# Kernel optimization log

Hardware: AMD Instinct MI355X
Metric: run time of the kernel (lower is better)

The kernel has to match this reference:

```python
import jax, jax.numpy as jnp
import numpy as np

MARGIN = 0.3   # init margin
NUMBER = 1024  # OHEM: number of hardest losses to mine
N, D = 8192, 128


def setup_inputs() -> dict:
    key = jax.random.key(0)
    k1, k2 = jax.random.split(key)
    pair1 = jax.random.normal(k1, (N, D), dtype=jnp.float32)
    pair2 = jax.random.normal(k2, (N, D), dtype=jnp.float32)
    return {"pair1": pair1, "pair2": pair2}


def _pairwise_losses(pair1, pair2):
    # d[i, j] = ||pair1[i] - pair2[j]||^2 via GEMM expansion
    sq1 = jnp.sum(pair1 * pair1, axis=1)            # [N]
    sq2 = jnp.sum(pair2 * pair2, axis=1)            # [N]
    cross = pair1 @ pair2.T                          # [N, N]
    d = sq1[:, None] + sq2[None, :] - 2.0 * cross    # [N, N]
    dist_ap = jnp.diagonal(d)                        # [N], ||pair1[i]-pair2[i]||^2
    loss = jax.nn.relu(dist_ap[:, None] - d + MARGIN)  # [N, N]
    offdiag = ~jnp.eye(d.shape[0], dtype=bool)       # i == j is skipped
    return loss, offdiag


def reference(pair1, pair2):
    loss, offdiag = _pairwise_losses(pair1, pair2)
    n = loss.shape[0]
    cnt = 2 * n * (n - 1)  # original appends each (i, j) loss twice
    # all_loss: mean over all 2*N*(N-1) (duplicated) losses
    all_loss = 2.0 * jnp.sum(jnp.where(offdiag, loss, 0.0)) / cnt
    # OHEM: top NUMBER losses over the duplicated candidate set
    flat = jnp.where(offdiag, loss, -1.0).ravel()    # sentinel -1 masks diagonal
    flat2 = jnp.concatenate([flat, flat])            # each loss appears twice
    topv, _ = jax.lax.top_k(flat2, NUMBER)
    pos = topv > 0.0
    avg_num = jnp.sum(pos)
    avg_sum = jnp.sum(jnp.where(pos, topv, 0.0))
    # if no positive loss among the mined set, fall back to the single largest loss
    avg_loss = jnp.where(avg_num > 0, avg_sum / jnp.maximum(avg_num, 1).astype(topv.dtype), topv[0])
    return avg_loss, all_loss
```

## Files before the change

kernel.cpp:

```cpp
#include <hip/hip_runtime.h>
#include <stdint.h>


#define NROWS 8192
#define DDIM  128
#define MARGIN_F 0.3f
#define HALFK 512
#define SUBCAP 8192
#define SHIST_BINS 1024

typedef unsigned short u16;
typedef short bf16x8 __attribute__((ext_vector_type(8)));
typedef float f32x4 __attribute__((ext_vector_type(4)));

#define OFF_P1B  0
#define OFF_P2B  (2*1024*1024)
#define OFF_AARR (4*1024*1024)
#define OFF_BARR (OFF_AARR + 32768)
#define OFF_MISC (OFF_AARR + 65536)
#define OFF_CAND (OFF_MISC + 8192)

__device__ __forceinline__ u16 f2bf(float f) {
    unsigned int u = __float_as_uint(f);
    u = (u + 0x7FFFu + ((u >> 16) & 1u)) >> 16;
    return (u16)u;
}
__device__ __forceinline__ float bf2f(u16 u) {
    return __uint_as_float(((unsigned int)u) << 16);
}

__global__ __launch_bounds__(256) void prep_kernel(
    const float* __restrict__ p1, const float* __restrict__ p2,
    u16* __restrict__ p1b, u16* __restrict__ p2b,
    float* __restrict__ aArr, float* __restrict__ bArr,
    int* __restrict__ misc)
{
    if (blockIdx.x == 0) {
        for (int i = threadIdx.x; i < 1232; i += 256) misc[i] = 0;
    }
    const int wid = threadIdx.x >> 6, lane = threadIdx.x & 63;
    const int row = blockIdx.x*4 + wid;
    const float2 v1 = *(const float2*)&p1[row*DDIM + lane*2];
    const float2 v2 = *(const float2*)&p2[row*DDIM + lane*2];
    p1b[row*DDIM + lane*2]     = f2bf(v1.x);
    p1b[row*DDIM + lane*2 + 1] = f2bf(v1.y);
    p2b[row*DDIM + lane*2]     = f2bf(v2.x);
    p2b[row*DDIM + lane*2 + 1] = f2bf(v2.y);
    float sq = v2.x*v2.x + v2.y*v2.y;
    float cp = v1.x*v2.x + v1.y*v2.y;
    #pragma unroll
    for (int off = 32; off > 0; off >>= 1) {
        sq += __shfl_down(sq, off);
        cp += __shfl_down(cp, off);
    }
    if (lane == 0) {
        bArr[row] = sq;
        aArr[row] = sq - 2.0f*cp + MARGIN_F;
    }
}

__global__ __launch_bounds__(256) void sample_kernel(
    const u16* __restrict__ p1b, const u16* __restrict__ p2b,
    const float* __restrict__ aArr, const float* __restrict__ bArr,
    int* __restrict__ shist)
{
    __shared__ float p1row[DDIM];
    __shared__ int h[SHIST_BINS];
    const int b = blockIdx.x;
    const int i = (b >> 3)*1024 + 512;
    const int j0 = (b & 7)*1024;
    const int tid = threadIdx.x;
    for (int k = tid; k < SHIST_BINS; k += 256) h[k] = 0;
    if (tid < DDIM) p1row[tid] = bf2f(p1b[i*DDIM + tid]);
    __syncthreads();
    const float ai = aArr[i];
    #pragma unroll
    for (int jj = 0; jj < 4; ++jj) {
        const int j = j0 + jj*256 + tid;
        const u16* prow = &p2b[j*DDIM];
        float dot = 0.f;
        for (int k = 0; k < DDIM; k += 8) {
            uint4 q = *(const uint4*)&prow[k];
            const u16* e = (const u16*)&q;
            #pragma unroll
            for (int t = 0; t < 8; ++t) dot += p1row[k + t] * bf2f(e[t]);
        }
        float v = ai - bArr[j] + 2.0f*dot;
        if (j != i && v > 0.f) {
            int bin = (int)(v * 4.0f);
            if (bin > SHIST_BINS - 1) bin = SHIST_BINS - 1;
            atomicAdd(&h[bin], 1);
        }
    }
    __syncthreads();
    for (int k = tid; k < SHIST_BINS; k += 256) if (h[k]) atomicAdd(&shist[k], h[k]);
}

__global__ __launch_bounds__(256) void pick_kernel(
    const int* __restrict__ shist, float* __restrict__ Tv)
{
    __shared__ int h[SHIST_BINS];
    __shared__ int chunk[256];
    const int tid = threadIdx.x;
    #pragma unroll
    for (int k = 0; k < 4; ++k) h[tid + k*256] = shist[tid + k*256];
    __syncthreads();
    int cs = 0;
    #pragma unroll
    for (int k = 0; k < 4; ++k) cs += h[tid*4 + k];
    chunk[tid] = cs;
    __syncthreads();
    if (tid == 0) {
        int run = 0, tc = -1;
        for (int t = 255; t >= 0; --t) {
            if (run + chunk[t] >= 8) { tc = t; break; }
            run += chunk[t];
        }
        float t0 = 0.f;
        if (tc >= 0) {
            int b = tc*4 + 3;
            for (; b >= tc*4; --b) { run += h[b]; if (run >= 8) break; }
            if (b < tc*4) b = tc*4;
            while (run > 24 && run - h[b] >= 8 && b < SHIST_BINS - 1) { run -= h[b]; b++; }
            t0 = 0.25f * (float)b;
        }
        *Tv = t0;
    }
}

__global__ __launch_bounds__(512, 4) void pair_gemm(
    const u16* __restrict__ p1b, const u16* __restrict__ p2b,
    const float* __restrict__ aArr, const float* __restrict__ bArr,
    const float* __restrict__ Tv,
    float* __restrict__ pS, int* __restrict__ pP,
    int* __restrict__ candCnt, float* __restrict__ cand)
{
    __shared__ u16 At[128][136];
    __shared__ u16 Bt[128][136];
    __shared__ float sredS[8];
    __shared__ int   sredP[8];
    const int tid = threadIdx.x;
    const int bi = blockIdx.y, bj = blockIdx.x;
    const int i0 = bi*128, j0 = bj*128;
    const float T0 = *Tv;
    #pragma unroll
    for (int it = 0; it < 4; ++it) {
        int c = tid + it*512;
        int r = c >> 4, cc = (c & 15) * 8;
        *(uint4*)&At[r][cc] = *(const uint4*)&p1b[(i0 + r)*DDIM + cc];
        *(uint4*)&Bt[r][cc] = *(const uint4*)&p2b[(j0 + r)*DDIM + cc];
    }
    __syncthreads();
    const int lane = tid & 63, wid = tid >> 6;
    const int r16 = lane & 15, hi = lane >> 4;
    const int wm = (wid >> 2)*64;
    const int wn = (wid & 3)*32;
    f32x4 acc[4][2];
    #pragma unroll
    for (int a = 0; a < 4; ++a)
        #pragma unroll
        for (int b = 0; b < 2; ++b) acc[a][b] = (f32x4){0.f, 0.f, 0.f, 0.f};
    #pragma unroll
    for (int ks = 0; ks < 4; ++ks) {
        const int kc = ks*32 + hi*8;
        bf16x8 aF[4], bF[2];
        #pragma unroll
        for (int mi = 0; mi < 4; ++mi) aF[mi] = *(const bf16x8*)&At[wm + mi*16 + r16][kc];
        #pragma unroll
        for (int ni = 0; ni < 2; ++ni) bF[ni] = *(const bf16x8*)&Bt[wn + ni*16 + r16][kc];
        #pragma unroll
        for (int mi = 0; mi < 4; ++mi)
            #pragma unroll
            for (int ni = 0; ni < 2; ++ni)
                acc[mi][ni] = __builtin_amdgcn_mfma_f32_16x16x32_bf16(aF[mi], bF[ni], acc[mi][ni], 0, 0, 0);
    }
    float bv[2], av[4][4];
    #pragma unroll
    for (int ni = 0; ni < 2; ++ni) bv[ni] = bArr[j0 + wn + ni*16 + r16];
    #pragma unroll
    for (int mi = 0; mi < 4; ++mi)
        #pragma unroll
        for (int r = 0; r < 4; ++r) av[mi][r] = aArr[i0 + wm + mi*16 + hi*4 + r];
    const int copy = (bi ^ bj) & 63;
    int*   myCnt  = &candCnt[copy];
    float* myCand = &cand[(size_t)copy * SUBCAP];
    float lsum = 0.f; int pcnt = 0;
    #pragma unroll
    for (int mi = 0; mi < 4; ++mi) {
        #pragma unroll
        for (int ni = 0; ni < 2; ++ni) {
            const bool hasDiag = (i0 + wm + mi*16) == (j0 + wn + ni*16);
            #pragma unroll
            for (int r = 0; r < 4; ++r) {
                const float v = av[mi][r] - bv[ni] + 2.0f*acc[mi][ni][r];
                lsum += fmaxf(v, 0.f);
                pcnt += (v > 0.f) ? 1 : 0;
                bool ok = (v >= T0);
                if (hasDiag && (hi*4 + r) == r16) ok = false;
                if (ok) {
                    int idx = atomicAdd(myCnt, 1);
                    if (idx < SUBCAP) myCand[idx] = v;
                }
            }
        }
    }
    #pragma unroll
    for (int off = 32; off > 0; off >>= 1) {
        lsum += __shfl_down(lsum, off);
        pcnt += __shfl_down(pcnt, off);
    }
    if (lane == 0) { sredS[wid] = lsum; sredP[wid] = pcnt; }
    __syncthreads();
    if (tid == 0) {
        float s = 0.f; int p = 0;
        #pragma unroll
        for (int w = 0; w < 8; ++w) { s += sredS[w]; p += sredP[w]; }
        atomicAdd(&pS[copy], s);
        atomicAdd(&pP[copy], p);
    }
}

__device__ __forceinline__ float block_reduce1024(float v, float* red, int tid) {
    #pragma unroll
    for (int off = 32; off > 0; off >>= 1) v += __shfl_down(v, off);
    __syncthreads();
    if ((tid & 63) == 0) red[tid >> 6] = v;
    __syncthreads();
    if (tid == 0) {
        float t = 0.f;
        #pragma unroll
        for (int w = 0; w < 16; ++w) t += red[w];
        red[0] = t;
    }
    __syncthreads();
    return red[0];
}

__global__ __launch_bounds__(1024) void select_kernel(
    const float* __restrict__ pS, const int* __restrict__ pP,
    const int* __restrict__ candCnt, const float* __restrict__ cand,
    const float* __restrict__ Tv, float* __restrict__ out)
{
    __shared__ int h1[1024];
    __shared__ int h2[1024];
    __shared__ float red[16];
    __shared__ int ints[8];
    __shared__ float fl[2];
    __shared__ float lst[4096];
    const int tid = threadIdx.x;
    for (int k = tid; k < 1024; k += 1024) { h1[k] = 0; h2[k] = 0; }
    if (tid == 0) {
        double sd = 0.0; int p = 0, c = 0;
        for (int k = 0; k < 64; ++k) {
            sd += (double)pS[k];
            p += pP[k];
            int cc = candCnt[k];
            c += (cc > SUBCAP ? SUBCAP : cc);
        }
        sd -= (double)NROWS * (double)MARGIN_F;
        if (sd < 0.0) sd = 0.0;
        p -= NROWS;
        if (p < 0) p = 0;
        ints[0] = p; ints[1] = c; ints[6] = 0;
        fl[0] = (float)sd;
    }
    __syncthreads();
    const int P = ints[0], C = ints[1];
    const float S = fl[0];
    const float all_loss = S * (1.0f / 67100672.0f);
    const float lo = *Tv;
    float avg = 0.f;

    if (P == 0) {
        avg = 0.f;
    } else if (P < HALFK) {
        avg = S / (float)P;
    } else if (C < HALFK) {
        float s = 0.f;
        for (int c = 0; c < 64; ++c) {
            int n = min(candCnt[c], SUBCAP);
            for (int k = tid; k < n; k += 1024) s += cand[(size_t)c*SUBCAP + k];
        }
        s = block_reduce1024(s, red, tid);
        avg = (C > 0) ? (s + (float)(HALFK - C)*lo) / (float)HALFK : 0.f;
    } else {
        for (int c = 0; c < 64; ++c) {
            int n = min(candCnt[c], SUBCAP);
            for (int k = tid; k < n; k += 1024) {
                float v = cand[(size_t)c*SUBCAP + k];
                int b = (int)((v - lo) * 0.25f);
                b = b < 0 ? 0 : (b > 1023 ? 1023 : b);
                atomicAdd(&h1[b], 1);
            }
        }
        __syncthreads();
        if (tid == 0) {
            int run = 0;
            for (int b = 1023; b >= 0; --b) {
                run += h1[b];
                if (run >= HALFK) { ints[2] = b; ints[3] = HALFK - (run - h1[b]); break; }
            }
        }
        __syncthreads();
        const int b1 = ints[2], needK = ints[3];
        const float lo2 = lo + (float)b1 * 4.0f;
        float s1 = 0.f;
        for (int c = 0; c < 64; ++c) {
            int n = min(candCnt[c], SUBCAP);
            for (int k = tid; k < n; k += 1024) {
                float v = cand[(size_t)c*SUBCAP + k];
                int b = (int)((v - lo) * 0.25f);
                b = b < 0 ? 0 : (b > 1023 ? 1023 : b);
                if (b > b1) s1 += v;
                else if (b == b1) {
                    int sb = (int)((v - lo2) * 256.0f);
                    sb = sb < 0 ? 0 : (sb > 1023 ? 1023 : sb);
                    atomicAdd(&h2[sb], 1);
                }
            }
        }
        s1 = block_reduce1024(s1, red, tid);
        if (tid == 0) {
            int run = 0;
            for (int b = 1023; b >= 0; --b) {
                run += h2[b];
                if (run >= needK) { ints[4] = b; ints[5] = needK - (run - h2[b]); break; }
            }
        }
        __syncthreads();
        const int b2 = ints[4], need3 = ints[5];
        float s2 = 0.f;
        for (int c = 0; c < 64; ++c) {
            int n = min(candCnt[c], SUBCAP);
            for (int k = tid; k < n; k += 1024) {
                float v = cand[(size_t)c*SUBCAP + k];
                int b = (int)((v - lo) * 0.25f);
                b = b < 0 ? 0 : (b > 1023 ? 1023 : b);
                if (b == b1) {
                    int sb = (int)((v - lo2) * 256.0f);
                    sb = sb < 0 ? 0 : (sb > 1023 ? 1023 : sb);
                    if (sb > b2) s2 += v;
                    else if (sb == b2) {
                        int idx = atomicAdd(&ints[6], 1);
                        if (idx < 4096) lst[idx] = v;
                    }
                }
            }
        }
        s2 = block_reduce1024(s2, red, tid);
        __syncthreads();
        const int m = min(ints[6], 4096);
        float s3 = 0.f;
        for (int k = tid; k < m; k += 1024) {
            float v = lst[k]; int g = 0;
            for (int j = 0; j < m; ++j) {
                float u = lst[j];
                g += (u > v) || (u == v && j < k);
            }
            if (g < need3) s3 += v;
        }
        s3 = block_reduce1024(s3, red, tid);
        avg = (s1 + s2 + s3) * (1.0f / (float)HALFK);
    }
    if (tid == 0) { out[0] = avg; out[1] = all_loss; }
}

extern "C" void kernel_launch(void* const* d_in, const int* in_sizes, int n_in,
                              void* d_out, int out_size, void* d_ws, size_t ws_size,
                              hipStream_t stream)
{
    const float* p1 = (const float*)d_in[0];
    const float* p2 = (const float*)d_in[1];
    char* ws = (char*)d_ws;
    u16*   p1b  = (u16*)(ws + OFF_P1B);
    u16*   p2b  = (u16*)(ws + OFF_P2B);
    float* aArr = (float*)(ws + OFF_AARR);
    float* bArr = (float*)(ws + OFF_BARR);
    int*   misc = (int*)(ws + OFF_MISC);
    int*   shist = misc;
    float* pS   = (float*)(misc + 1024);
    int*   pP   = misc + 1088;
    int*   cCnt = misc + 1152;
    float* Tv   = (float*)(misc + 1216);
    float* cand = (float*)(ws + OFF_CAND);
    float* out  = (float*)d_out;

    prep_kernel<<<NROWS/4, 256, 0, stream>>>(p1, p2, p1b, p2b, aArr, bArr, misc);
    sample_kernel<<<64, 256, 0, stream>>>(p1b, p2b, aArr, bArr, shist);
    pick_kernel<<<1, 256, 0, stream>>>(shist, Tv);
    dim3 grid(64, 64);
    pair_gemm<<<grid, 512, 0, stream>>>(p1b, p2b, aArr, bArr, Tv, pS, pP, cCnt, cand);
    select_kernel<<<1, 1024, 0, stream>>>(pS, pP, cCnt, cand, Tv, out);
}
```

Before: 375.1 us.

## Fuse launches via last-block tickets and convert fp32 to bf16 inside the GEMM

Removes the separate bf16 conversion pass: the GEMM tiles now load fp32 inputs and round to bf16 while staging into shared memory, and the sampler reads fp32 directly. The pick kernel is folded into the sampler and the select kernel into the GEMM, each using an atomic ticket so the last finishing block runs the tail work, cutting two launches. The trade-off is double the global read bytes per GEMM tile, conversion work repeated by every tile, and a tail selection that now runs with 512 threads inside a register-constrained GEMM block.

```diff
diff --git a/kernel.cpp b/kernel.cpp
--- a/kernel.cpp
+++ b/kernel.cpp
@@ -8,13 +8,13 @@
 #define HALFK 512
 #define SUBCAP 8192
 #define SHIST_BINS 1024
+#define TICK_SAMP 1220
+#define TICK_GEMM 1224
 
 typedef unsigned short u16;
 typedef short bf16x8 __attribute__((ext_vector_type(8)));
 typedef float f32x4 __attribute__((ext_vector_type(4)));
 
-#define OFF_P1B  0
-#define OFF_P2B  (2*1024*1024)
 #define OFF_AARR (4*1024*1024)
 #define OFF_BARR (OFF_AARR + 32768)
 #define OFF_MISC (OFF_AARR + 65536)
@@ -25,65 +25,60 @@
     u = (u + 0x7FFFu + ((u >> 16) & 1u)) >> 16;
     return (u16)u;
 }
-__device__ __forceinline__ float bf2f(u16 u) {
-    return __uint_as_float(((unsigned int)u) << 16);
-}
 
 __global__ __launch_bounds__(256) void prep_kernel(
     const float* __restrict__ p1, const float* __restrict__ p2,
-    u16* __restrict__ p1b, u16* __restrict__ p2b,
-    float* __restrict__ aArr, float* __restrict__ bArr,
-    int* __restrict__ misc)
+    float* __restrict__ aArr, float* __restrict__ bArr, int* __restrict__ misc)
 {
     if (blockIdx.x == 0) {
         for (int i = threadIdx.x; i < 1232; i += 256) misc[i] = 0;
     }
-    const int wid = threadIdx.x >> 6, lane = threadIdx.x & 63;
-    const int row = blockIdx.x*4 + wid;
-    const float2 v1 = *(const float2*)&p1[row*DDIM + lane*2];
-    const float2 v2 = *(const float2*)&p2[row*DDIM + lane*2];
-    p1b[row*DDIM + lane*2]     = f2bf(v1.x);
-    p1b[row*DDIM + lane*2 + 1] = f2bf(v1.y);
-    p2b[row*DDIM + lane*2]     = f2bf(v2.x);
-    p2b[row*DDIM + lane*2 + 1] = f2bf(v2.y);
-    float sq = v2.x*v2.x + v2.y*v2.y;
-    float cp = v1.x*v2.x + v1.y*v2.y;
-    #pragma unroll
-    for (int off = 32; off > 0; off >>= 1) {
-        sq += __shfl_down(sq, off);
-        cp += __shfl_down(cp, off);
-    }
-    if (lane == 0) {
-        bArr[row] = sq;
-        aArr[row] = sq - 2.0f*cp + MARGIN_F;
-    }
-}
-
-__global__ __launch_bounds__(256) void sample_kernel(
-    const u16* __restrict__ p1b, const u16* __restrict__ p2b,
+    const int w = threadIdx.x >> 6, lane = threadIdx.x & 63;
+    #pragma unroll
+    for (int k = 0; k < 4; ++k) {
+        const int row = blockIdx.x*16 + w*4 + k;
+        const float2 v1 = *(const float2*)&p1[row*DDIM + lane*2];
+        const float2 v2 = *(const float2*)&p2[row*DDIM + lane*2];
+        float sq = v2.x*v2.x + v2.y*v2.y;
+        float cp = v1.x*v2.x + v1.y*v2.y;
+        #pragma unroll
+        for (int off = 32; off > 0; off >>= 1) {
+            sq += __shfl_down(sq, off);
+            cp += __shfl_down(cp, off);
+        }
+        if (lane == 0) {
+            bArr[row] = sq;
+            aArr[row] = sq - 2.0f*cp + MARGIN_F;
+        }
+    }
+}
+
+__global__ __launch_bounds__(256) void sample_pick(
+    const float* __restrict__ p1, const float* __restrict__ p2,
     const float* __restrict__ aArr, const float* __restrict__ bArr,
-    int* __restrict__ shist)
+    int* __restrict__ misc, float* __restrict__ Tv)
 {
     __shared__ float p1row[DDIM];
     __shared__ int h[SHIST_BINS];
+    __shared__ int chunk[256];
+    __shared__ int lastFlag;
+    int* shist = misc;
     const int b = blockIdx.x;
     const int i = (b >> 3)*1024 + 512;
     const int j0 = (b & 7)*1024;
     const int tid = threadIdx.x;
     for (int k = tid; k < SHIST_BINS; k += 256) h[k] = 0;
-    if (tid < DDIM) p1row[tid] = bf2f(p1b[i*DDIM + tid]);
+    if (tid < DDIM) p1row[tid] = p1[i*DDIM + tid];
     __syncthreads();
     const float ai = aArr[i];
     #pragma unroll
     for (int jj = 0; jj < 4; ++jj) {
         const int j = j0 + jj*256 + tid;
-        const u16* prow = &p2b[j*DDIM];
+        const float* prow = &p2[j*DDIM];
         float dot = 0.f;
-        for (int k = 0; k < DDIM; k += 8) {
-            uint4 q = *(const uint4*)&prow[k];
-            const u16* e = (const u16*)&q;
-            #pragma unroll
-            for (int t = 0; t < 8; ++t) dot += p1row[k + t] * bf2f(e[t]);
+        for (int k = 0; k < DDIM; k += 4) {
+            float4 q = *(const float4*)&prow[k];
+            dot += p1row[k]*q.x + p1row[k+1]*q.y + p1row[k+2]*q.z + p1row[k+3]*q.w;
         }
         float v = ai - bArr[j] + 2.0f*dot;
         if (j != i && v > 0.f) {
@@ -94,16 +89,18 @@
     }
     __syncthreads();
     for (int k = tid; k < SHIST_BINS; k += 256) if (h[k]) atomicAdd(&shist[k], h[k]);
-}
-
-__global__ __launch_bounds__(256) void pick_kernel(
-    const int* __restrict__ shist, float* __restrict__ Tv)
-{
-    __shared__ int h[SHIST_BINS];
-    __shared__ int chunk[256];
-    const int tid = threadIdx.x;
-    #pragma unroll
-    for (int k = 0; k < 4; ++k) h[tid + k*256] = shist[tid + k*256];
+    __threadfence();
+    if (tid == 0) {
+        int t = __hip_atomic_fetch_add(misc + TICK_SAMP, 1, __ATOMIC_ACQ_REL,
+                                       __HIP_MEMORY_SCOPE_AGENT);
+        lastFlag = (t == 63);
+    }
+    __syncthreads();
+    if (!lastFlag) return;
+    #pragma unroll
+    for (int k = 0; k < 4; ++k)
+        h[tid + k*256] = __hip_atomic_load(&shist[tid + k*256], __ATOMIC_RELAXED,
+                                           __HIP_MEMORY_SCOPE_AGENT);
     __syncthreads();
     int cs = 0;
     #pragma unroll
@@ -118,37 +115,64 @@
         }
         float t0 = 0.f;
         if (tc >= 0) {
-            int b = tc*4 + 3;
-            for (; b >= tc*4; --b) { run += h[b]; if (run >= 8) break; }
-            if (b < tc*4) b = tc*4;
-            while (run > 24 && run - h[b] >= 8 && b < SHIST_BINS - 1) { run -= h[b]; b++; }
-            t0 = 0.25f * (float)b;
+            int b2 = tc*4 + 3;
+            for (; b2 >= tc*4; --b2) { run += h[b2]; if (run >= 8) break; }
+            if (b2 < tc*4) b2 = tc*4;
+            while (run > 24 && run - h[b2] >= 8 && b2 < SHIST_BINS - 1) { run -= h[b2]; b2++; }
+            t0 = 0.25f * (float)b2;
         }
         *Tv = t0;
     }
 }
 
-__global__ __launch_bounds__(512, 4) void pair_gemm(
-    const u16* __restrict__ p1b, const u16* __restrict__ p2b,
+__device__ __forceinline__ float blk_reduce512(float v, volatile float* red, int tid) {
+    #pragma unroll
+    for (int off = 32; off > 0; off >>= 1) v += __shfl_down(v, off);
+    __syncthreads();
+    if ((tid & 63) == 0) red[tid >> 6] = v;
+    __syncthreads();
+    if (tid == 0) {
+        float t = 0.f;
+        #pragma unroll
+        for (int w = 0; w < 8; ++w) t += red[w];
+        red[0] = t;
+    }
+    __syncthreads();
+    float r = red[0];
+    __syncthreads();
+    return r;
+}
+
+__global__ __launch_bounds__(512, 4) void gemm_select(
+    const float* __restrict__ p1, const float* __restrict__ p2,
     const float* __restrict__ aArr, const float* __restrict__ bArr,
     const float* __restrict__ Tv,
     float* __restrict__ pS, int* __restrict__ pP,
-    int* __restrict__ candCnt, float* __restrict__ cand)
+    int* __restrict__ candCnt, float* __restrict__ cand,
+    int* __restrict__ misc, float* __restrict__ out)
 {
     __shared__ u16 At[128][136];
     __shared__ u16 Bt[128][136];
     __shared__ float sredS[8];
     __shared__ int   sredP[8];
+    __shared__ int   lastFlag;
     const int tid = threadIdx.x;
     const int bi = blockIdx.y, bj = blockIdx.x;
     const int i0 = bi*128, j0 = bj*128;
     const float T0 = *Tv;
     #pragma unroll
-    for (int it = 0; it < 4; ++it) {
-        int c = tid + it*512;
-        int r = c >> 4, cc = (c & 15) * 8;
-        *(uint4*)&At[r][cc] = *(const uint4*)&p1b[(i0 + r)*DDIM + cc];
-        *(uint4*)&Bt[r][cc] = *(const uint4*)&p2b[(j0 + r)*DDIM + cc];
+    for (int it = 0; it < 8; ++it) {
+        int f = tid + it*512;
+        int r = f >> 5, c4 = f & 31;
+        float4 qa = *(const float4*)&p1[(i0 + r)*DDIM + c4*4];
+        float4 qb = *(const float4*)&p2[(j0 + r)*DDIM + c4*4];
+        uint2 ua, ub;
+        ua.x = (unsigned)f2bf(qa.x) | ((unsigned)f2bf(qa.y) << 16);
+        ua.y = (unsigned)f2bf(qa.z) | ((unsigned)f2bf(qa.w) << 16);
+        ub.x = (unsigned)f2bf(qb.x) | ((unsigned)f2bf(qb.y) << 16);
+        ub.y = (unsigned)f2bf(qb.z) | ((unsigned)f2bf(qb.w) << 16);
+        *(uint2*)&At[r][c4*4] = ua;
+        *(uint2*)&Bt[r][c4*4] = ub;
     }
     __syncthreads();
     const int lane = tid & 63, wid = tid >> 6;
@@ -218,43 +242,38 @@
         atomicAdd(&pS[copy], s);
         atomicAdd(&pP[copy], p);
     }
-}
-
-__device__ __forceinline__ float block_reduce1024(float v, float* red, int tid) {
-    #pragma unroll
-    for (int off = 32; off > 0; off >>= 1) v += __shfl_down(v, off);
-    __syncthreads();
-    if ((tid & 63) == 0) red[tid >> 6] = v;
-    __syncthreads();
-    if (tid == 0) {
-        float t = 0.f;
-        #pragma unroll
-        for (int w = 0; w < 16; ++w) t += red[w];
-        red[0] = t;
-    }
-    __syncthreads();
-    return red[0];
-}
-
-__global__ __launch_bounds__(1024) void select_kernel(
-    const float* __restrict__ pS, const int* __restrict__ pP,
-    const int* __restrict__ candCnt, const float* __restrict__ cand,
-    const float* __restrict__ Tv, float* __restrict__ out)
-{
-    __shared__ int h1[1024];
-    __shared__ int h2[1024];
-    __shared__ float red[16];
-    __shared__ int ints[8];
-    __shared__ float fl[2];
-    __shared__ float lst[4096];
-    const int tid = threadIdx.x;
-    for (int k = tid; k < 1024; k += 1024) { h1[k] = 0; h2[k] = 0; }
+    __threadfence();
+    if (tid == 0) {
+        int t = __hip_atomic_fetch_add(misc + TICK_GEMM, 1, __ATOMIC_ACQ_REL,
+                                       __HIP_MEMORY_SCOPE_AGENT);
+        lastFlag = (t == 64*64 - 1);
+    }
+    __syncthreads();
+    if (!lastFlag) return;
+
+    char* smem = (char*)&At[0][0];
+    int*   h1  = (int*)smem;
+    int*   h2  = (int*)(smem + 4096);
+    float* lst = (float*)(smem + 8192);
+    volatile float* red = (float*)(smem + 24576);
+    int*   ints = (int*)(smem + 24640);
+    float* fl  = (float*)(smem + 24704);
+    float* spS = (float*)(smem + 24768);
+    int*   spP = (int*)(smem + 25024);
+    int*   sCC = (int*)(smem + 25280);
+    for (int k = tid; k < 1024; k += 512) { h1[k] = 0; h2[k] = 0; }
+    if (tid < 64) {
+        spS[tid] = __hip_atomic_load(&pS[tid], __ATOMIC_RELAXED, __HIP_MEMORY_SCOPE_AGENT);
+        spP[tid] = __hip_atomic_load(&pP[tid], __ATOMIC_RELAXED, __HIP_MEMORY_SCOPE_AGENT);
+        sCC[tid] = __hip_atomic_load(&candCnt[tid], __ATOMIC_RELAXED, __HIP_MEMORY_SCOPE_AGENT);
+    }
+    __syncthreads();
     if (tid == 0) {
         double sd = 0.0; int p = 0, c = 0;
         for (int k = 0; k < 64; ++k) {
-            sd += (double)pS[k];
-            p += pP[k];
-            int cc = candCnt[k];
+            sd += (double)spS[k];
+            p += spP[k];
+            int cc = sCC[k];
             c += (cc > SUBCAP ? SUBCAP : cc);
         }
         sd -= (double)NROWS * (double)MARGIN_F;
@@ -268,8 +287,11 @@
     const int P = ints[0], C = ints[1];
     const float S = fl[0];
     const float all_loss = S * (1.0f / 67100672.0f);
-    const float lo = *Tv;
+    const float lo = T0;
     float avg = 0.f;
+
+    #define CLOAD(c, k) __hip_atomic_load(&cand[(size_t)(c)*SUBCAP + (k)], \
+                         __ATOMIC_RELAXED, __HIP_MEMORY_SCOPE_AGENT)
 
     if (P == 0) {
         avg = 0.f;
@@ -278,16 +300,16 @@
     } else if (C < HALFK) {
         float s = 0.f;
         for (int c = 0; c < 64; ++c) {
-            int n = min(candCnt[c], SUBCAP);
-            for (int k = tid; k < n; k += 1024) s += cand[(size_t)c*SUBCAP + k];
-        }
-        s = block_reduce1024(s, red, tid);
+            int n = min(sCC[c], SUBCAP);
+            for (int k = tid; k < n; k += 512) s += CLOAD(c, k);
+        }
+        s = blk_reduce512(s, red, tid);
         avg = (C > 0) ? (s + (float)(HALFK - C)*lo) / (float)HALFK : 0.f;
     } else {
         for (int c = 0; c < 64; ++c) {
-            int n = min(candCnt[c], SUBCAP);
-            for (int k = tid; k < n; k += 1024) {
-                float v = cand[(size_t)c*SUBCAP + k];
+            int n = min(sCC[c], SUBCAP);
+            for (int k = tid; k < n; k += 512) {
+                float v = CLOAD(c, k);
                 int b = (int)((v - lo) * 0.25f);
                 b = b < 0 ? 0 : (b > 1023 ? 1023 : b);
                 atomicAdd(&h1[b], 1);
@@ -306,9 +328,9 @@
         const float lo2 = lo + (float)b1 * 4.0f;
         float s1 = 0.f;
         for (int c = 0; c < 64; ++c) {
-            int n = min(candCnt[c], SUBCAP);
-            for (int k = tid; k < n; k += 1024) {
-                float v = cand[(size_t)c*SUBCAP + k];
+            int n = min(sCC[c], SUBCAP);
+            for (int k = tid; k < n; k += 512) {
+                float v = CLOAD(c, k);
                 int b = (int)((v - lo) * 0.25f);
                 b = b < 0 ? 0 : (b > 1023 ? 1023 : b);
                 if (b > b1) s1 += v;
@@ -319,7 +341,7 @@
                 }
             }
         }
-        s1 = block_reduce1024(s1, red, tid);
+        s1 = blk_reduce512(s1, red, tid);
         if (tid == 0) {
             int run = 0;
             for (int b = 1023; b >= 0; --b) {
@@ -331,9 +353,9 @@
         const int b2 = ints[4], need3 = ints[5];
         float s2 = 0.f;
         for (int c = 0; c < 64; ++c) {
-            int n = min(candCnt[c], SUBCAP);
-            for (int k = tid; k < n; k += 1024) {
-                float v = cand[(size_t)c*SUBCAP + k];
+            int n = min(sCC[c], SUBCAP);
+            for (int k = tid; k < n; k += 512) {
+                float v = CLOAD(c, k);
                 int b = (int)((v - lo) * 0.25f);
                 b = b < 0 ? 0 : (b > 1023 ? 1023 : b);
                 if (b == b1) {
@@ -347,11 +369,11 @@
                 }
             }
         }
-        s2 = block_reduce1024(s2, red, tid);
+        s2 = blk_reduce512(s2, red, tid);
         __syncthreads();
         const int m = min(ints[6], 4096);
         float s3 = 0.f;
-        for (int k = tid; k < m; k += 1024) {
+        for (int k = tid; k < m; k += 512) {
             float v = lst[k]; int g = 0;
             for (int j = 0; j < m; ++j) {
                 float u = lst[j];
@@ -359,10 +381,11 @@
             }
             if (g < need3) s3 += v;
         }
-        s3 = block_reduce1024(s3, red, tid);
+        s3 = blk_reduce512(s3, red, tid);
         avg = (s1 + s2 + s3) * (1.0f / (float)HALFK);
     }
     if (tid == 0) { out[0] = avg; out[1] = all_loss; }
+    #undef CLOAD
 }
 
 extern "C" void kernel_launch(void* const* d_in, const int* in_sizes, int n_in,
@@ -372,12 +395,9 @@
     const float* p1 = (const float*)d_in[0];
     const float* p2 = (const float*)d_in[1];
     char* ws = (char*)d_ws;
-    u16*   p1b  = (u16*)(ws + OFF_P1B);
-    u16*   p2b  = (u16*)(ws + OFF_P2B);
     float* aArr = (float*)(ws + OFF_AARR);
     float* bArr = (float*)(ws + OFF_BARR);
     int*   misc = (int*)(ws + OFF_MISC);
-    int*   shist = misc;
     float* pS   = (float*)(misc + 1024);
     int*   pP   = misc + 1088;
     int*   cCnt = misc + 1152;
@@ -385,10 +405,8 @@
     float* cand = (float*)(ws + OFF_CAND);
     float* out  = (float*)d_out;
 
-    prep_kernel<<<NROWS/4, 256, 0, stream>>>(p1, p2, p1b, p2b, aArr, bArr, misc);
-    sample_kernel<<<64, 256, 0, stream>>>(p1b, p2b, aArr, bArr, shist);
-    pick_kernel<<<1, 256, 0, stream>>>(shist, Tv);
+    prep_kernel<<<512, 256, 0, stream>>>(p1, p2, aArr, bArr, misc);
+    sample_pick<<<64, 256, 0, stream>>>(p1, p2, aArr, bArr, misc, Tv);
     dim3 grid(64, 64);
-    pair_gemm<<<grid, 512, 0, stream>>>(p1b, p2b, aArr, bArr, Tv, pS, pP, cCnt, cand);
-    select_kernel<<<1, 1024, 0, stream>>>(pS, pP, cCnt, cand, Tv, out);
-}
+    gemm_select<<<grid, 512, 0, stream>>>(p1, p2, aArr, bArr, Tv, pS, pP, cCnt, cand, misc, out);
+}
```

Result: slower. 986.8 us (+163.1%).
